# Optimization experiments

Hardware: AMD Instinct MI355X
Metric: run time of the kernel (lower is better)

## Reference

```python
import jax, jax.numpy as jnp
import numpy as np

B, V, T = 256, 128000, 16
TOP_K = 100          # min(100, V - n_targets) == 100 since V >> T
TARGET_MARGIN = 1.0
EPS = 1e-8
NEG = -1e30          # sentinel so masked target slots never enter top-k


def setup_inputs() -> dict:
    key = jax.random.key(0)
    k1, k2 = jax.random.split(key)
    # Non-negative sparse activations (SPLADE-style relu output) in [0,1)
    sparse_rep = jax.random.uniform(k1, (B, V), dtype=jnp.float32)
    # Fixed-length padded target id lists (all rows valid -> n_valid = B)
    target_ids = jax.random.randint(k2, (B, T), 0, V).astype(jnp.int64)
    return {"sparse_rep": sparse_rep, "target_ids": target_ids}


def reference(sparse_rep, target_ids):
    # [B, T] gather of target activations (one batched gather, no per-row loop)
    tgt = jnp.take_along_axis(sparse_rep, target_ids, axis=1)
    # -log(a + eps), per-row mean then batch mean == global mean (fixed T)
    target_loss = -jnp.mean(jnp.log(tgt + EPS))
    # hinge margin on target activations
    margin_loss = jnp.mean(jax.nn.relu(TARGET_MARGIN - tgt))
    # mask out target columns per row, then top-k over remaining vocab
    rows = jnp.arange(sparse_rep.shape[0])[:, None]          # [B, 1]
    masked = sparse_rep.at[rows, target_ids].set(NEG)        # [B, V]
    top_vals = jax.lax.top_k(masked, TOP_K)[0]               # [B, TOP_K]
    negative_loss = jnp.mean(top_vals)
    return (target_loss, margin_loss, negative_loss)
```

## Files before the change

### kernel.cpp

```cpp
#include <hip/hip_runtime.h>
#include <cstddef>
#include <cstdint>

#define B_    256
#define V_    128000
#define T_    16
#define TOPK_ 100
#define TPB   1024
#define CAP   4096
#define NF4   (V_ / 4)
#define NHIST 4096

__global__ void zero_out_kernel(float* o) {
    o[0] = 0.f; o[1] = 0.f; o[2] = 0.f;
}

__global__ __launch_bounds__(TPB) void row_kernel(
        const float* __restrict__ sparse,
        const int*   __restrict__ tids,
        float*       __restrict__ out) {
    __shared__ float    s_cand[CAP];
    __shared__ unsigned s_hist[NHIST];
    __shared__ int      s_ids[T_];
    __shared__ int      s_cnt;
    __shared__ int      s_bstar;
    __shared__ float    s_red[128];

    const int row = blockIdx.x;
    const int tid = threadIdx.x;
    const float* __restrict__ rp = sparse + (size_t)row * V_;

    if (tid < T_) s_ids[tid] = tids[row * T_ + tid];
    if (tid == 0) s_cnt = 0;
    __syncthreads();

    if (tid < T_) {
        float x  = rp[s_ids[tid]];
        float tl = -logf(x + 1e-8f);
        float ml = fmaxf(1.0f - x, 0.0f);
        #pragma unroll
        for (int off = 8; off > 0; off >>= 1) {
            tl += __shfl_down(tl, off);
            ml += __shfl_down(ml, off);
        }
        if (tid == 0) {
            atomicAdd(out + 0, tl * (1.0f / (B_ * T_)));
            atomicAdd(out + 1, ml * (1.0f / (B_ * T_)));
        }
    }

    const float4* rp4 = (const float4*)rp;
    const float T0 = 0.996f;
    for (int i = tid; i < NF4; i += TPB) {
        float4 v = rp4[i];
        int col = i << 2;
        float xs[4] = {v.x, v.y, v.z, v.w};
        #pragma unroll
        for (int c = 0; c < 4; ++c) {
            float x = xs[c];
            if (x >= T0) {
                int cc = col + c;
                bool is_t = false;
                #pragma unroll
                for (int j = 0; j < T_; ++j) is_t |= (cc == s_ids[j]);
                if (!is_t) {
                    int k = atomicAdd(&s_cnt, 1);
                    if (k < CAP) s_cand[k] = x;
                }
            }
        }
    }
    __syncthreads();

    int cnt = s_cnt;

    if (cnt < TOPK_ || cnt > CAP) {
        for (int i = tid; i < NHIST; i += TPB) s_hist[i] = 0u;
        __syncthreads();
        for (int i = tid; i < NF4; i += TPB) {
            float4 v = rp4[i];
            float xs[4] = {v.x, v.y, v.z, v.w};
            #pragma unroll
            for (int c = 0; c < 4; ++c) {
                int b = (int)(xs[c] * (float)NHIST);
                b = min(max(b, 0), NHIST - 1);
                atomicAdd(&s_hist[b], 1u);
            }
        }
        __syncthreads();
        if (tid == 0) {
            for (int j = 0; j < T_; ++j) {
                int id = s_ids[j];
                bool dup = false;
                for (int q = 0; q < j; ++q) dup = dup || (s_ids[q] == id);
                if (!dup) {
                    int b = (int)(rp[id] * (float)NHIST);
                    b = min(max(b, 0), NHIST - 1);
                    s_hist[b]--;
                }
            }
            int acc = 0, b = NHIST - 1;
            for (; b >= 0; --b) {
                acc += (int)s_hist[b];
                if (acc >= TOPK_) break;
            }
            s_bstar = max(b, 0);
            s_cnt = 0;
        }
        __syncthreads();
        int bstar = s_bstar;
        for (int i = tid; i < NF4; i += TPB) {
            float4 v = rp4[i];
            int col = i << 2;
            float xs[4] = {v.x, v.y, v.z, v.w};
            #pragma unroll
            for (int c = 0; c < 4; ++c) {
                float x = xs[c];
                int b = (int)(x * (float)NHIST);
                b = min(max(b, 0), NHIST - 1);
                if (b >= bstar) {
                    int cc = col + c;
                    bool is_t = false;
                    #pragma unroll
                    for (int j = 0; j < T_; ++j) is_t |= (cc == s_ids[j]);
                    if (!is_t) {
                        int k = atomicAdd(&s_cnt, 1);
                        if (k < CAP) s_cand[k] = x;
                    }
                }
            }
        }
        __syncthreads();
        cnt = min(s_cnt, CAP);
    }

    int n2 = 128;
    while (n2 < cnt) n2 <<= 1;
    for (int i = cnt + tid; i < n2; i += TPB) s_cand[i] = -1e30f;
    __syncthreads();

    for (int k = 2; k <= n2; k <<= 1) {
        for (int j = k >> 1; j > 0; j >>= 1) {
            for (int i = tid; i < n2; i += TPB) {
                int p = i ^ j;
                if (p > i) {
                    float a = s_cand[i], b = s_cand[p];
                    bool asc = ((i & k) == 0);
                    if (asc ? (a > b) : (a < b)) {
                        s_cand[i] = b; s_cand[p] = a;
                    }
                }
            }
            __syncthreads();
        }
    }

    if (tid < 128) {
        float v = (tid < TOPK_) ? s_cand[n2 - 1 - tid] : 0.f;
        s_red[tid] = v;
    }
    __syncthreads();
    #pragma unroll
    for (int off = 64; off > 0; off >>= 1) {
        if (tid < off) s_red[tid] += s_red[tid + off];
        __syncthreads();
    }
    if (tid == 0) atomicAdd(out + 2, s_red[0] * (1.0f / (B_ * TOPK_)));
}

extern "C" void kernel_launch(void* const* d_in, const int* in_sizes, int n_in,
                              void* d_out, int out_size, void* d_ws, size_t ws_size,
                              hipStream_t stream) {
    const float* sparse = (const float*)d_in[0];
    const int*   tids   = (const int*)d_in[1];
    float*       out    = (float*)d_out;

    zero_out_kernel<<<1, 1, 0, stream>>>(out);
    row_kernel<<<B_, TPB, 0, stream>>>(sparse, tids, out);
}
```

Baseline: 209.1 us.

## Split row scan across slices and replace bitonic sort with rank-based top-k

The candidate-collection pass is moved into its own kernel that gives each row 8 blocks of 256 threads, each scanning one slice and appending candidates above a raised threshold to a global workspace through global atomics. A second kernel per row loads the candidates, keeps the histogram fallback, and replaces the bitonic sort with an all-pairs rank count that sums values ranked below 100. The aim is more memory-level parallelism across the GPU for the bandwidth-bound scan and fewer barrier-heavy sort passes. The cost is an extra kernel launch, global atomic contention per row, and a quadratic rank loop that depends on the candidate count.

```diff
diff --git a/kernel.cpp b/kernel.cpp
--- a/kernel.cpp
+++ b/kernel.cpp
@@ -2,36 +2,81 @@
 #include <cstddef>
 #include <cstdint>
 
-#define B_    256
-#define V_    128000
-#define T_    16
-#define TOPK_ 100
-#define TPB   1024
-#define CAP   4096
-#define NF4   (V_ / 4)
-#define NHIST 4096
+#define B_     256
+#define V_     128000
+#define T_     16
+#define TOPK_  100
+#define CAP    4096
+#define NF4    (V_ / 4)
+#define NHIST  4096
+#define SLICES 8
+#define F4S    (NF4 / SLICES)
+#define T0     0.998f
 
-__global__ void zero_out_kernel(float* o) {
-    o[0] = 0.f; o[1] = 0.f; o[2] = 0.f;
+
+__global__ void zero_kernel(float* o, int* ws_cnt) {
+    int t = threadIdx.x;
+    if (t < 3) o[t] = 0.f;
+    if (t < B_) ws_cnt[t] = 0;
 }
 
-__global__ __launch_bounds__(TPB) void row_kernel(
+__global__ __launch_bounds__(256) void collect_kernel(
         const float* __restrict__ sparse,
         const int*   __restrict__ tids,
+        float*       __restrict__ ws_cand,
+        int*         __restrict__ ws_cnt) {
+    __shared__ int s_ids[T_];
+    const int blk = blockIdx.x;
+    const int row = blk >> 3;
+    const int sl  = blk & (SLICES - 1);
+    const int tid = threadIdx.x;
+    if (tid < T_) s_ids[tid] = tids[row * T_ + tid];
+    __syncthreads();
+
+    const float4* __restrict__ rp4 = (const float4*)(sparse + (size_t)row * V_);
+    float* __restrict__ cand = ws_cand + (size_t)row * CAP;
+    int*   cntp = ws_cnt + row;
+
+    const int i0 = sl * F4S;
+    for (int i = i0 + tid; i < i0 + F4S; i += 256) {
+        float4 v = rp4[i];
+        int col = i << 2;
+        float xs[4] = {v.x, v.y, v.z, v.w};
+        #pragma unroll
+        for (int c = 0; c < 4; ++c) {
+            float x = xs[c];
+            if (x >= T0) {
+                int cc = col + c;
+                bool is_t = false;
+                #pragma unroll
+                for (int j = 0; j < T_; ++j) is_t |= (cc == s_ids[j]);
+                if (!is_t) {
+                    int k = atomicAdd(cntp, 1);
+                    if (k < CAP) cand[k] = x;
+                }
+            }
+        }
+    }
+}
+
+__global__ __launch_bounds__(256) void reduce_kernel(
+        const float* __restrict__ sparse,
+        const int*   __restrict__ tids,
+        const float* __restrict__ ws_cand,
+        const int*   __restrict__ ws_cnt,
         float*       __restrict__ out) {
     __shared__ float    s_cand[CAP];
     __shared__ unsigned s_hist[NHIST];
     __shared__ int      s_ids[T_];
     __shared__ int      s_cnt;
     __shared__ int      s_bstar;
-    __shared__ float    s_red[128];
+    __shared__ float    s_red[4];
 
     const int row = blockIdx.x;
     const int tid = threadIdx.x;
     const float* __restrict__ rp = sparse + (size_t)row * V_;
 
     if (tid < T_) s_ids[tid] = tids[row * T_ + tid];
-    if (tid == 0) s_cnt = 0;
     __syncthreads();
 
     if (tid < T_) {
@@ -49,35 +94,18 @@
         }
     }
 
-    const float4* rp4 = (const float4*)rp;
-    const float T0 = 0.996f;
-    for (int i = tid; i < NF4; i += TPB) {
-        float4 v = rp4[i];
-        int col = i << 2;
-        float xs[4] = {v.x, v.y, v.z, v.w};
-        #pragma unroll
-        for (int c = 0; c < 4; ++c) {
-            float x = xs[c];
-            if (x >= T0) {
-                int cc = col + c;
-                bool is_t = false;
-                #pragma unroll
-                for (int j = 0; j < T_; ++j) is_t |= (cc == s_ids[j]);
-                if (!is_t) {
-                    int k = atomicAdd(&s_cnt, 1);
-                    if (k < CAP) s_cand[k] = x;
-                }
-            }
-        }
-    }
-    __syncthreads();
+    int cnt = ws_cnt[row];
 
-    int cnt = s_cnt;
-
-    if (cnt < TOPK_ || cnt > CAP) {
-        for (int i = tid; i < NHIST; i += TPB) s_hist[i] = 0u;
+    if (cnt >= TOPK_ && cnt <= CAP) {
+        const float* cand = ws_cand + (size_t)row * CAP;
+        for (int i = tid; i < cnt; i += 256) s_cand[i] = cand[i];
         __syncthreads();
-        for (int i = tid; i < NF4; i += TPB) {
+    } else {
+        for (int i = tid; i < NHIST; i += 256) s_hist[i] = 0u;
+        if (tid == 0) s_cnt = 0;
+        __syncthreads();
+        const float4* rp4 = (const float4*)rp;
+        for (int i = tid; i < NF4; i += 256) {
             float4 v = rp4[i];
             float xs[4] = {v.x, v.y, v.z, v.w};
             #pragma unroll
@@ -105,11 +133,10 @@
                 if (acc >= TOPK_) break;
             }
             s_bstar = max(b, 0);
-            s_cnt = 0;
         }
         __syncthreads();
         int bstar = s_bstar;
-        for (int i = tid; i < NF4; i += TPB) {
+        for (int i = tid; i < NF4; i += 256) {
             float4 v = rp4[i];
             int col = i << 2;
             float xs[4] = {v.x, v.y, v.z, v.w};
@@ -134,38 +161,25 @@
         cnt = min(s_cnt, CAP);
     }
 
-    int n2 = 128;
-    while (n2 < cnt) n2 <<= 1;
-    for (int i = cnt + tid; i < n2; i += TPB) s_cand[i] = -1e30f;
-    __syncthreads();
-
-    for (int k = 2; k <= n2; k <<= 1) {
-        for (int j = k >> 1; j > 0; j >>= 1) {
-            for (int i = tid; i < n2; i += TPB) {
-                int p = i ^ j;
-                if (p > i) {
-                    float a = s_cand[i], b = s_cand[p];
-                    bool asc = ((i & k) == 0);
-                    if (asc ? (a > b) : (a < b)) {
-                        s_cand[i] = b; s_cand[p] = a;
-                    }
-                }
-            }
-            __syncthreads();
+    float sum = 0.f;
+    for (int i = tid; i < cnt; i += 256) {
+        float x = s_cand[i];
+        int rank = 0;
+        for (int j = 0; j < cnt; ++j) {
+            float y = s_cand[j];
+            rank += (y > x) ? 1 : ((y == x && j < i) ? 1 : 0);
         }
+        if (rank < TOPK_) sum += x;
     }
 
-    if (tid < 128) {
-        float v = (tid < TOPK_) ? s_cand[n2 - 1 - tid] : 0.f;
-        s_red[tid] = v;
+    #pragma unroll
+    for (int off = 32; off > 0; off >>= 1) sum += __shfl_down(sum, off);
+    if ((tid & 63) == 0) s_red[tid >> 6] = sum;
+    __syncthreads();
+    if (tid == 0) {
+        float tot = s_red[0] + s_red[1] + s_red[2] + s_red[3];
+        atomicAdd(out + 2, tot * (1.0f / (B_ * TOPK_)));
     }
-    __syncthreads();
-    #pragma unroll
-    for (int off = 64; off > 0; off >>= 1) {
-        if (tid < off) s_red[tid] += s_red[tid + off];
-        __syncthreads();
-    }
-    if (tid == 0) atomicAdd(out + 2, s_red[0] * (1.0f / (B_ * TOPK_)));
 }
 
 extern "C" void kernel_launch(void* const* d_in, const int* in_sizes, int n_in,
@@ -174,7 +188,10 @@
     const float* sparse = (const float*)d_in[0];
     const int*   tids   = (const int*)d_in[1];
     float*       out    = (float*)d_out;
+    int*         ws_cnt  = (int*)d_ws;
+    float*       ws_cand = (float*)((char*)d_ws + 4096);
 
-    zero_out_kernel<<<1, 1, 0, stream>>>(out);
-    row_kernel<<<B_, TPB, 0, stream>>>(sparse, tids, out);
+    zero_kernel<<<1, 256, 0, stream>>>(out, ws_cnt);
+    collect_kernel<<<B_ * SLICES, 256, 0, stream>>>(sparse, tids, ws_cand, ws_cnt);
+    reduce_kernel<<<B_, 256, 0, stream>>>(sparse, tids, ws_cand, ws_cnt, out);
 }
```

Result: slower. 245.7 us (+17.5%).
